# Optimization experiments

Hardware: AMD Instinct MI355X
Metric: run time of the kernel (lower is better)

Reference implementation:

```python
import jax, jax.numpy as jnp
import numpy as np

DIM = 3072
HEADS = 24
HEAD_DIM = 128
INNER = HEADS * HEAD_DIM
EPS = 1e-6
B, IMG_LEN, TXT_LEN = 1, 2048, 512
S = IMG_LEN + TXT_LEN


def setup_inputs() -> dict:
    key = jax.random.key(0)
    ks = jax.random.split(key, 16)
    w = lambda k, shp: (jax.random.normal(k, shp, dtype=jnp.float32) * 0.02)
    return {
        "x": jax.random.normal(ks[0], (B, IMG_LEN, DIM), dtype=jnp.float32),
        "ctx": jax.random.normal(ks[1], (B, TXT_LEN, DIM), dtype=jnp.float32),
        "rope_cos": jax.random.uniform(ks[2], (S, HEAD_DIM), dtype=jnp.float32),
        "rope_sin": jax.random.uniform(ks[3], (S, HEAD_DIM), dtype=jnp.float32),
        "wq": w(ks[4], (INNER, DIM)),
        "wk": w(ks[5], (INNER, DIM)),
        "wv": w(ks[6], (INNER, DIM)),
        "gq": jnp.ones((HEAD_DIM,), jnp.float32),
        "gk": jnp.ones((HEAD_DIM,), jnp.float32),
        "wo": w(ks[7], (DIM, INNER)),
        "awq": w(ks[8], (INNER, DIM)),
        "awk": w(ks[9], (INNER, DIM)),
        "awv": w(ks[10], (INNER, DIM)),
        "agq": jnp.ones((HEAD_DIM,), jnp.float32),
        "agk": jnp.ones((HEAD_DIM,), jnp.float32),
        "awo": w(ks[11], (DIM, INNER)),
    }


def _rms_norm(t, g):
    # t: [b, s, h, d]; normalize over last dim
    var = jnp.mean(t * t, axis=-1, keepdims=True)
    return t * jax.lax.rsqrt(var + EPS) * g


def _heads(t):
    # [b, s, h*d] -> [b, s, h, d]
    b, s, _ = t.shape
    return t.reshape(b, s, HEADS, HEAD_DIM)


def _apply_rope(t, cos, sin):
    # t: [b, s, h, d]; cos/sin: [s, d] interleaved-pair layout (diffusers Flux style)
    b, s, h, d = t.shape
    x = t.reshape(b, s, h, d // 2, 2)
    rot = jnp.stack([-x[..., 1], x[..., 0]], axis=-1).reshape(b, s, h, d)
    c = cos[None, :, None, :]
    si = sin[None, :, None, :]
    return t * c + rot * si


def reference(x, ctx, rope_cos, rope_sin, wq, wk, wv, gq, gk, wo,
              awq, awk, awv, agq, agk, awo):
    # image-stream QKV + per-head RMSNorm on q,k
    q = _rms_norm(_heads(x @ wq.T), gq)
    k = _rms_norm(_heads(x @ wk.T), gk)
    v = _heads(x @ wv.T)
    # context-stream QKV
    qc = _rms_norm(_heads(ctx @ awq.T), agq)
    kc = _rms_norm(_heads(ctx @ awk.T), agk)
    vc = _heads(ctx @ awv.T)
    # joint streams: [ctx, img] ordering (out[:, :txt_len] is context)
    q = jnp.concatenate([qc, q], axis=1)
    k = jnp.concatenate([kc, k], axis=1)
    v = jnp.concatenate([vc, v], axis=1)
    q = _apply_rope(q, rope_cos, rope_sin)
    k = _apply_rope(k, rope_cos, rope_sin)
    # SDPA
    scale = 1.0 / jnp.sqrt(jnp.float32(HEAD_DIM))
    scores = jnp.einsum('bqhd,bkhd->bhqk', q, k) * scale
    probs = jax.nn.softmax(scores, axis=-1)
    out = jnp.einsum('bhqk,bkhd->bqhd', probs, v)
    out = out.reshape(out.shape[0], out.shape[1], INNER)
    img_out = out[:, TXT_LEN:] @ wo.T
    txt_out = out[:, :TXT_LEN] @ awo.T
    return (img_out, txt_out)
```

## Files before the change

kernel.cpp:

```cpp
#include <hip/hip_runtime.h>
#include <hip/hip_bf16.h>

#define DIMC 3072
#define NHEADS 24
#define HD 128
#define SEQ 2560
#define TXTLEN 512
#define IMGLEN 2048

using short8 = __attribute__((ext_vector_type(8))) short;
using f32x4  = __attribute__((ext_vector_type(4))) float;

static __device__ __forceinline__ float bf2f(unsigned short u) {
    unsigned v = ((unsigned)u) << 16;
    return __builtin_bit_cast(float, v);
}
static __device__ __forceinline__ unsigned short f2bf(float f) {
    unsigned u = __builtin_bit_cast(unsigned, f);
    return (unsigned short)((u + 0x7FFFu + ((u >> 16) & 1u)) >> 16);
}
static __device__ __forceinline__ void gload16(const void* g, void* l) {
    __builtin_amdgcn_global_load_lds((const __attribute__((address_space(1))) unsigned int*)g,
                                     (__attribute__((address_space(3))) unsigned int*)l,
                                     16, 0, 0);
}

__global__ __launch_bounds__(256)
void castk(const float* __restrict__ in, unsigned short* __restrict__ out, int n8)
{
    const int i = blockIdx.x * 256 + threadIdx.x;
    if (i >= n8) return;
    const float4 a = *reinterpret_cast<const float4*>(in + (size_t)i * 8);
    const float4 b = *reinterpret_cast<const float4*>(in + (size_t)i * 8 + 4);
    short8 o;
    o[0] = (short)f2bf(a.x); o[1] = (short)f2bf(a.y);
    o[2] = (short)f2bf(a.z); o[3] = (short)f2bf(a.w);
    o[4] = (short)f2bf(b.x); o[5] = (short)f2bf(b.y);
    o[6] = (short)f2bf(b.z); o[7] = (short)f2bf(b.w);
    *reinterpret_cast<short8*>(out + (size_t)i * 8) = o;
}

struct W8 { const float* src[8]; };
__global__ __launch_bounds__(256)
void castw(W8 a, unsigned short* __restrict__ dstbase, int n8, size_t wsz)
{
    const int i = blockIdx.x * 256 + threadIdx.x;
    if (i >= n8) return;
    const float* in = a.src[blockIdx.y];
    unsigned short* out = dstbase + (size_t)blockIdx.y * wsz;
    const float4 av = *reinterpret_cast<const float4*>(in + (size_t)i * 8);
    const float4 bv = *reinterpret_cast<const float4*>(in + (size_t)i * 8 + 4);
    short8 o;
    o[0] = (short)f2bf(av.x); o[1] = (short)f2bf(av.y);
    o[2] = (short)f2bf(av.z); o[3] = (short)f2bf(av.w);
    o[4] = (short)f2bf(bv.x); o[5] = (short)f2bf(bv.y);
    o[6] = (short)f2bf(bv.z); o[7] = (short)f2bf(bv.w);
    *reinterpret_cast<short8*>(out + (size_t)i * 8) = o;
}

struct QkvArgs {
    const unsigned short* A;
    const unsigned short* w0[3];
    const unsigned short* w1[3];
    unsigned short* c[3];
    const float *gq, *gk, *agq, *agk, *rc, *rs;
};

__global__ __launch_bounds__(256)
void gemm_qkv(QkvArgs args)
{
    __shared__ unsigned short As[128 * 32];
    __shared__ unsigned short Bs[128 * 32];

    const int bm = blockIdx.x;
    int bn = blockIdx.y;
    const int which = bn / 24; bn -= which * 24;
    const int rowbase = bm * 128, colbase = bn * 128;
    const unsigned short* __restrict__ A = args.A;
    const unsigned short* __restrict__ W = (rowbase < TXTLEN) ? args.w0[which] : args.w1[which];
    unsigned short* __restrict__ C = args.c[which];

    const int t = threadIdx.x, w = t >> 6, l = t & 63;
    const int lr = l & 15, lk = l >> 4;

    f32x4 acc[2][8] = {};

    const unsigned short* Ag = A + (size_t)(rowbase + w * 32 + (l >> 2)) * DIMC + (l & 3) * 8;
    const unsigned short* Wg = W + (size_t)(colbase + w * 32 + (l >> 2)) * DIMC + (l & 3) * 8;
    unsigned short* AsB = &As[w * 1024];
    unsigned short* BsB = &Bs[w * 1024];

    for (int k0 = 0; k0 < DIMC; k0 += 32) {
        gload16(Ag + k0,             AsB);
        gload16(Ag + 16 * DIMC + k0, AsB + 512);
        gload16(Wg + k0,             BsB);
        gload16(Wg + 16 * DIMC + k0, BsB + 512);
        __syncthreads();
        short8 af[2], bf[8];
#pragma unroll
        for (int m = 0; m < 2; ++m)
            af[m] = *reinterpret_cast<const short8*>(&As[(w * 32 + m * 16 + lr) * 32 + lk * 8]);
#pragma unroll
        for (int n = 0; n < 8; ++n)
            bf[n] = *reinterpret_cast<const short8*>(&Bs[(n * 16 + lr) * 32 + lk * 8]);
#pragma unroll
        for (int m = 0; m < 2; ++m)
#pragma unroll
            for (int n = 0; n < 8; ++n)
                acc[m][n] = __builtin_amdgcn_mfma_f32_16x16x32_bf16(af[m], bf[n], acc[m][n], 0, 0, 0);
        __syncthreads();
    }

    if (which < 2) {
        const float* gg = (which == 0) ? ((rowbase < TXTLEN) ? args.agq : args.gq)
                                       : ((rowbase < TXTLEN) ? args.agk : args.gk);
        const float qscale = (which == 0) ? 0.08838834764831845f : 1.0f;
        float gcol[8];
#pragma unroll
        for (int n = 0; n < 8; ++n) gcol[n] = gg[n * 16 + lr];

#pragma unroll
        for (int m = 0; m < 2; ++m) {
#pragma unroll
            for (int r = 0; r < 4; ++r) {
                const int srow = rowbase + w * 32 + m * 16 + lk * 4 + r;
                float ss = 0.f;
#pragma unroll
                for (int n = 0; n < 8; ++n) ss += acc[m][n][r] * acc[m][n][r];
#pragma unroll
                for (int off = 1; off < 16; off <<= 1) ss += __shfl_xor(ss, off);
                const float rn = rsqrtf(ss * (1.f / HD) + 1e-6f);
                unsigned short* crow = C + (size_t)srow * DIMC + colbase;
                const float* crs = args.rc + (size_t)srow * HD;
                const float* srs = args.rs + (size_t)srow * HD;
#pragma unroll
                for (int n = 0; n < 8; ++n) {
                    const int col = n * 16 + lr;
                    const float v = acc[m][n][r] * rn * gcol[n];
                    const float pv = __shfl_xor(v, 1);
                    const float o = (v * crs[col] + ((lr & 1) ? pv : -pv) * srs[col]) * qscale;
                    crow[col] = f2bf(o);
                }
            }
        }
    } else {
#pragma unroll
        for (int m = 0; m < 2; ++m) {
#pragma unroll
            for (int r = 0; r < 4; ++r) {
                const int srow = rowbase + w * 32 + m * 16 + lk * 4 + r;
                unsigned short* crow = C + (size_t)srow * DIMC + colbase;
#pragma unroll
                for (int n = 0; n < 8; ++n)
                    crow[n * 16 + lr] = f2bf(acc[m][n][r]);
            }
        }
    }
}

__global__ __launch_bounds__(256)
void gemm_out(const unsigned short* __restrict__ A, const unsigned short* __restrict__ W0,
              const unsigned short* __restrict__ W1, float* __restrict__ Ctxt,
              float* __restrict__ Cimg)
{
    __shared__ unsigned short As[128 * 32];
    __shared__ unsigned short Bs[128 * 32];

    const int bm = blockIdx.x, bn = blockIdx.y;
    const int rowbase = bm * 128, colbase = bn * 128;
    const unsigned short* __restrict__ W = (rowbase < TXTLEN) ? W0 : W1;

    const int t = threadIdx.x, w = t >> 6, l = t & 63;
    const int lr = l & 15, lk = l >> 4;
    const int wr = (w >> 1) * 64, wc = (w & 1) * 64;

    f32x4 acc[4][4] = {};

    const unsigned short* Ag = A + (size_t)(rowbase + w * 32 + (l >> 2)) * DIMC + (l & 3) * 8;
    const unsigned short* Wg = W + (size_t)(colbase + w * 32 + (l >> 2)) * DIMC + (l & 3) * 8;
    unsigned short* AsB = &As[w * 1024];
    unsigned short* BsB = &Bs[w * 1024];

    for (int k0 = 0; k0 < DIMC; k0 += 32) {
        gload16(Ag + k0,             AsB);
        gload16(Ag + 16 * DIMC + k0, AsB + 512);
        gload16(Wg + k0,             BsB);
        gload16(Wg + 16 * DIMC + k0, BsB + 512);
        __syncthreads();
        short8 af[4], bf[4];
#pragma unroll
        for (int m = 0; m < 4; ++m)
            af[m] = *reinterpret_cast<const short8*>(&As[(wr + m * 16 + lr) * 32 + lk * 8]);
#pragma unroll
        for (int n = 0; n < 4; ++n)
            bf[n] = *reinterpret_cast<const short8*>(&Bs[(wc + n * 16 + lr) * 32 + lk * 8]);
#pragma unroll
        for (int m = 0; m < 4; ++m)
#pragma unroll
            for (int n = 0; n < 4; ++n)
                acc[m][n] = __builtin_amdgcn_mfma_f32_16x16x32_bf16(af[m], bf[n], acc[m][n], 0, 0, 0);
        __syncthreads();
    }

    float* Cb; int rloc;
    if (rowbase < TXTLEN) { Cb = Ctxt; rloc = rowbase; }
    else                  { Cb = Cimg; rloc = rowbase - TXTLEN; }
#pragma unroll
    for (int m = 0; m < 4; ++m) {
#pragma unroll
        for (int r = 0; r < 4; ++r) {
            const int row = rloc + wr + m * 16 + lk * 4 + r;
            float* crow = Cb + (size_t)row * DIMC + colbase + wc;
#pragma unroll
            for (int n = 0; n < 4; ++n)
                crow[n * 16 + lr] = acc[m][n][r];
        }
    }
}

__global__ __launch_bounds__(256)
void transpose_v(const unsigned short* __restrict__ V, unsigned short* __restrict__ Vt)
{
    __shared__ unsigned short Ts[64][136];
    const int kt = blockIdx.x, h = blockIdx.y;
    const int t = threadIdx.x;
#pragma unroll
    for (int p = 0; p < 4; ++p) {
        const int row = p * 16 + (t >> 4);
        const int col = (t & 15) * 8;
        *reinterpret_cast<short8*>(&Ts[row][col]) =
            *reinterpret_cast<const short8*>(V + (size_t)(kt * 64 + row) * DIMC + h * HD + col);
    }
    __syncthreads();
    const int d = t >> 1, kh = t & 1;
    unsigned short* dst = Vt + (size_t)h * HD * SEQ + (size_t)d * SEQ + kt * 64 + kh * 32;
#pragma unroll
    for (int j4 = 0; j4 < 4; ++j4) {
        short8 o;
#pragma unroll
        for (int j = 0; j < 8; ++j) o[j] = (short)Ts[kh * 32 + j4 * 8 + j][d];
        *reinterpret_cast<short8*>(dst + j4 * 8) = o;
    }
}

__global__ __launch_bounds__(512)
void attn_mfma(const unsigned short* __restrict__ Q, const unsigned short* __restrict__ K,
               const unsigned short* __restrict__ Vt, unsigned short* __restrict__ O)
{
    __shared__ unsigned short Ks[2][64 * 128];
    __shared__ unsigned short Vs[2][128 * 64];
    __shared__ unsigned short Ps[8][16 * 64];

    const int bq = blockIdx.x, h = blockIdx.y;
    const int t = threadIdx.x, w = t >> 6, l = t & 63;
    const int lr = l & 15, lk = l >> 4;
    const int q0 = bq * 128 + w * 16;

    short8 qf[4];
#pragma unroll
    for (int kk = 0; kk < 4; ++kk)
        qf[kk] = *reinterpret_cast<const short8*>(
            Q + (size_t)(q0 + lr) * DIMC + h * HD + kk * 32 + lk * 8);

    f32x4 oacc[8] = {};
    float mrow[4] = {-1e30f, -1e30f, -1e30f, -1e30f};
    float lrow[4] = {};

    const unsigned short* Kg[2];
    const unsigned short* Vg[2];
    int krow_[2], vrow_[2];
#pragma unroll
    for (int i = 0; i < 2; ++i) {
        const int kr = w * 8 + i * 4 + (l >> 4);
        krow_[i] = kr;
        Kg[i] = K + (size_t)kr * DIMC + h * HD + (((l & 15) ^ (kr & 7)) * 8);
        const int vr = w * 16 + i * 8 + (l >> 3);
        vrow_[i] = vr;
        Vg[i] = Vt + (size_t)h * HD * SEQ + (size_t)vr * SEQ + (((l & 7) ^ (vr & 7)) * 8);
    }

    auto STAGE = [&](int buf, int kv0) {
#pragma unroll
        for (int i = 0; i < 2; ++i) {
            gload16(Kg[i] + (size_t)kv0 * DIMC, &Ks[buf][(w * 8 + i * 4) * 128]);
            gload16(Vg[i] + kv0,                &Vs[buf][(w * 16 + i * 8) * 64]);
        }
    };

    STAGE(0, 0);

    constexpr int NT = SEQ / 64;
    for (int kt = 0; kt < NT; ++kt) {
        const int buf = kt & 1;
        __syncthreads();
        if (kt + 1 < NT) STAGE(buf ^ 1, (kt + 1) * 64);

        f32x4 sf[4] = {};
#pragma unroll
        for (int nf = 0; nf < 4; ++nf) {
            const int row = nf * 16 + lr;
            const int sw = (row & 7) << 3;
#pragma unroll
            for (int kk = 0; kk < 4; ++kk) {
                short8 bfr = *reinterpret_cast<const short8*>(
                    &Ks[buf][row * 128 + ((kk * 32 + lk * 8) ^ sw)]);
                sf[nf] = __builtin_amdgcn_mfma_f32_16x16x32_bf16(qf[kk], bfr, sf[nf], 0, 0, 0);
            }
        }

        float alpha[4];
#pragma unroll
        for (int r = 0; r < 4; ++r) {
            float mx = fmaxf(fmaxf(sf[0][r], sf[1][r]), fmaxf(sf[2][r], sf[3][r]));
#pragma unroll
            for (int off = 1; off < 16; off <<= 1) mx = fmaxf(mx, __shfl_xor(mx, off));
            const float mn = fmaxf(mrow[r], mx);
            alpha[r] = __expf(mrow[r] - mn);
            mrow[r] = mn;
            float ps = 0.f;
#pragma unroll
            for (int nf = 0; nf < 4; ++nf) {
                const float p = __expf(sf[nf][r] - mn);
                sf[nf][r] = p;
                ps += p;
            }
#pragma unroll
            for (int off = 1; off < 16; off <<= 1) ps += __shfl_xor(ps, off);
            lrow[r] = lrow[r] * alpha[r] + ps;
        }
#pragma unroll
        for (int nf = 0; nf < 8; ++nf)
#pragma unroll
            for (int r = 0; r < 4; ++r) oacc[nf][r] *= alpha[r];

#pragma unroll
        for (int r = 0; r < 4; ++r) {
            const int prow = lk * 4 + r;
            const int sw = (prow & 7) << 3;
#pragma unroll
            for (int nf = 0; nf < 4; ++nf) {
                const int col = nf * 16 + lr;
                Ps[w][prow * 64 + (col ^ sw)] = f2bf(sf[nf][r]);
            }
        }

#pragma unroll
        for (int ks = 0; ks < 2; ++ks) {
            short8 pa = *reinterpret_cast<const short8*>(
                &Ps[w][lr * 64 + ((ks * 32 + lk * 8) ^ ((lr & 7) << 3))]);
#pragma unroll
            for (int nf = 0; nf < 8; ++nf) {
                const int vrow = nf * 16 + lr;
                short8 vf = *reinterpret_cast<const short8*>(
                    &Vs[buf][vrow * 64 + ((ks * 32 + lk * 8) ^ ((vrow & 7) << 3))]);
                oacc[nf] = __builtin_amdgcn_mfma_f32_16x16x32_bf16(pa, vf, oacc[nf], 0, 0, 0);
            }
        }
    }

    float inv[4];
#pragma unroll
    for (int r = 0; r < 4; ++r) inv[r] = 1.f / lrow[r];
#pragma unroll
    for (int nf = 0; nf < 8; ++nf)
#pragma unroll
        for (int r = 0; r < 4; ++r)
            O[(size_t)(q0 + lk * 4 + r) * DIMC + h * HD + nf * 16 + lr] = f2bf(oacc[nf][r] * inv[r]);
}

extern "C" void kernel_launch(void* const* d_in, const int* in_sizes, int n_in,
                              void* d_out, int out_size, void* d_ws, size_t ws_size,
                              hipStream_t stream)
{
    const float* x    = (const float*)d_in[0];
    const float* ctx  = (const float*)d_in[1];
    const float* rc   = (const float*)d_in[2];
    const float* rs   = (const float*)d_in[3];
    const float* wq   = (const float*)d_in[4];
    const float* wk   = (const float*)d_in[5];
    const float* wv   = (const float*)d_in[6];
    const float* gq   = (const float*)d_in[7];
    const float* gk   = (const float*)d_in[8];
    const float* wo   = (const float*)d_in[9];
    const float* awq  = (const float*)d_in[10];
    const float* awk  = (const float*)d_in[11];
    const float* awv  = (const float*)d_in[12];
    const float* agq  = (const float*)d_in[13];
    const float* agk  = (const float*)d_in[14];
    const float* awo  = (const float*)d_in[15];

    unsigned short* wsp = (unsigned short*)d_ws;
    const size_t SZ  = (size_t)SEQ * DIMC;
    const size_t WSZ = (size_t)DIMC * DIMC;
    unsigned short* XC  = wsp;
    unsigned short* Qb  = XC + SZ;
    unsigned short* Kb  = Qb + SZ;
    unsigned short* Vb  = Kb + SZ;
    unsigned short* Vtb = Vb + SZ;
    unsigned short* Ob  = Vtb + SZ;
    unsigned short* Wc  = Ob + SZ;

    {
        int n8 = (int)((size_t)TXTLEN * DIMC / 8);
        castk<<<dim3((n8 + 255) / 256), dim3(256), 0, stream>>>(ctx, XC, n8);
        n8 = (int)((size_t)IMGLEN * DIMC / 8);
        castk<<<dim3((n8 + 255) / 256), dim3(256), 0, stream>>>(x, XC + (size_t)TXTLEN * DIMC, n8);
    }
    {
        W8 w8;
        w8.src[0] = awq; w8.src[1] = wq; w8.src[2] = awk; w8.src[3] = wk;
        w8.src[4] = awv; w8.src[5] = wv; w8.src[6] = awo; w8.src[7] = wo;
        const int n8 = (int)(WSZ / 8);
        castw<<<dim3((n8 + 255) / 256, 8), dim3(256), 0, stream>>>(w8, Wc, n8, WSZ);
    }

    QkvArgs qa;
    qa.A = XC;
    qa.w0[0] = Wc + 0 * WSZ; qa.w1[0] = Wc + 1 * WSZ; qa.c[0] = Qb;
    qa.w0[1] = Wc + 2 * WSZ; qa.w1[1] = Wc + 3 * WSZ; qa.c[1] = Kb;
    qa.w0[2] = Wc + 4 * WSZ; qa.w1[2] = Wc + 5 * WSZ; qa.c[2] = Vb;
    qa.gq = gq; qa.gk = gk; qa.agq = agq; qa.agk = agk; qa.rc = rc; qa.rs = rs;
    gemm_qkv<<<dim3(SEQ / 128, 72), dim3(256), 0, stream>>>(qa);

    transpose_v<<<dim3(SEQ / 64, NHEADS), dim3(256), 0, stream>>>(Vb, Vtb);

    attn_mfma<<<dim3(SEQ / 128, NHEADS), dim3(512), 0, stream>>>(Qb, Kb, Vtb, Ob);

    float* out = (float*)d_out;
    gemm_out<<<dim3(SEQ / 128, DIMC / 128), dim3(256), 0, stream>>>(
        Ob, Wc + 6 * WSZ, Wc + 7 * WSZ, out + (size_t)IMGLEN * DIMC, out);
}
```

Baseline: 642.9 us.

## Double-buffer GEMMs, swizzle block order, split norm/RoPE into separate kernel

Both GEMMs now use double-buffered LDS staging, issuing the next K-slice load before computing the current one, and drop one barrier per iteration. Launches become 1D grids with an XCD-aware swizzle of block indices to improve L2 locality. The QKV GEMM switches to a 2x2 warp tiling and moves per-head RMSNorm and RoPE into a new normrope kernel, which adds an extra read/write pass over Q and K. The attention kernel wraps its MFMA sections in s_setprio to favour matrix issue.

After: 588.6 us. 8.5% less time.

```diff
diff --git a/kernel.cpp b/kernel.cpp
--- a/kernel.cpp
+++ b/kernel.cpp
@@ -63,18 +63,20 @@
     const unsigned short* w0[3];
     const unsigned short* w1[3];
     unsigned short* c[3];
-    const float *gq, *gk, *agq, *agk, *rc, *rs;
 };
 
 __global__ __launch_bounds__(256)
 void gemm_qkv(QkvArgs args)
 {
-    __shared__ unsigned short As[128 * 32];
-    __shared__ unsigned short Bs[128 * 32];
-
-    const int bm = blockIdx.x;
-    int bn = blockIdx.y;
+    __shared__ unsigned short As[2][128 * 32];
+    __shared__ unsigned short Bs[2][128 * 32];
+
+    const int bid = blockIdx.x;
+    const int swz = (bid & 7) * 180 + (bid >> 3);
+    const int bm = swz % 20;
+    int bn = swz / 20;
     const int which = bn / 24; bn -= which * 24;
+
     const int rowbase = bm * 128, colbase = bn * 128;
     const unsigned short* __restrict__ A = args.A;
     const unsigned short* __restrict__ W = (rowbase < TXTLEN) ? args.w0[which] : args.w1[which];
@@ -82,78 +84,51 @@
 
     const int t = threadIdx.x, w = t >> 6, l = t & 63;
     const int lr = l & 15, lk = l >> 4;
-
-    f32x4 acc[2][8] = {};
+    const int wr = (w >> 1) * 64, wc = (w & 1) * 64;
+
+    f32x4 acc[4][4] = {};
 
     const unsigned short* Ag = A + (size_t)(rowbase + w * 32 + (l >> 2)) * DIMC + (l & 3) * 8;
     const unsigned short* Wg = W + (size_t)(colbase + w * 32 + (l >> 2)) * DIMC + (l & 3) * 8;
-    unsigned short* AsB = &As[w * 1024];
-    unsigned short* BsB = &Bs[w * 1024];
-
-    for (int k0 = 0; k0 < DIMC; k0 += 32) {
-        gload16(Ag + k0,             AsB);
-        gload16(Ag + 16 * DIMC + k0, AsB + 512);
-        gload16(Wg + k0,             BsB);
-        gload16(Wg + 16 * DIMC + k0, BsB + 512);
+
+    auto STAGE = [&](int buf, int k0) {
+        gload16(Ag + k0,             &As[buf][w * 1024]);
+        gload16(Ag + 16 * DIMC + k0, &As[buf][w * 1024 + 512]);
+        gload16(Wg + k0,             &Bs[buf][w * 1024]);
+        gload16(Wg + 16 * DIMC + k0, &Bs[buf][w * 1024 + 512]);
+    };
+
+    STAGE(0, 0);
+
+    constexpr int NIT = DIMC / 32;
+    for (int it = 0; it < NIT; ++it) {
+        const int buf = it & 1;
         __syncthreads();
-        short8 af[2], bf[8];
-#pragma unroll
-        for (int m = 0; m < 2; ++m)
-            af[m] = *reinterpret_cast<const short8*>(&As[(w * 32 + m * 16 + lr) * 32 + lk * 8]);
-#pragma unroll
-        for (int n = 0; n < 8; ++n)
-            bf[n] = *reinterpret_cast<const short8*>(&Bs[(n * 16 + lr) * 32 + lk * 8]);
-#pragma unroll
-        for (int m = 0; m < 2; ++m)
-#pragma unroll
-            for (int n = 0; n < 8; ++n)
+        if (it + 1 < NIT) STAGE(buf ^ 1, (it + 1) * 32);
+
+        short8 af[4], bf[4];
+#pragma unroll
+        for (int m = 0; m < 4; ++m)
+            af[m] = *reinterpret_cast<const short8*>(&As[buf][(wr + m * 16 + lr) * 32 + lk * 8]);
+#pragma unroll
+        for (int n = 0; n < 4; ++n)
+            bf[n] = *reinterpret_cast<const short8*>(&Bs[buf][(wc + n * 16 + lr) * 32 + lk * 8]);
+#pragma unroll
+        for (int m = 0; m < 4; ++m)
+#pragma unroll
+            for (int n = 0; n < 4; ++n)
                 acc[m][n] = __builtin_amdgcn_mfma_f32_16x16x32_bf16(af[m], bf[n], acc[m][n], 0, 0, 0);
-        __syncthreads();
-    }
-
-    if (which < 2) {
-        const float* gg = (which == 0) ? ((rowbase < TXTLEN) ? args.agq : args.gq)
-                                       : ((rowbase < TXTLEN) ? args.agk : args.gk);
-        const float qscale = (which == 0) ? 0.08838834764831845f : 1.0f;
-        float gcol[8];
-#pragma unroll
-        for (int n = 0; n < 8; ++n) gcol[n] = gg[n * 16 + lr];
-
-#pragma unroll
-        for (int m = 0; m < 2; ++m) {
-#pragma unroll
-            for (int r = 0; r < 4; ++r) {
-                const int srow = rowbase + w * 32 + m * 16 + lk * 4 + r;
-                float ss = 0.f;
-#pragma unroll
-                for (int n = 0; n < 8; ++n) ss += acc[m][n][r] * acc[m][n][r];
-#pragma unroll
-                for (int off = 1; off < 16; off <<= 1) ss += __shfl_xor(ss, off);
-                const float rn = rsqrtf(ss * (1.f / HD) + 1e-6f);
-                unsigned short* crow = C + (size_t)srow * DIMC + colbase;
-                const float* crs = args.rc + (size_t)srow * HD;
-                const float* srs = args.rs + (size_t)srow * HD;
-#pragma unroll
-                for (int n = 0; n < 8; ++n) {
-                    const int col = n * 16 + lr;
-                    const float v = acc[m][n][r] * rn * gcol[n];
-                    const float pv = __shfl_xor(v, 1);
-                    const float o = (v * crs[col] + ((lr & 1) ? pv : -pv) * srs[col]) * qscale;
-                    crow[col] = f2bf(o);
-                }
-            }
-        }
-    } else {
-#pragma unroll
-        for (int m = 0; m < 2; ++m) {
-#pragma unroll
-            for (int r = 0; r < 4; ++r) {
-                const int srow = rowbase + w * 32 + m * 16 + lk * 4 + r;
-                unsigned short* crow = C + (size_t)srow * DIMC + colbase;
-#pragma unroll
-                for (int n = 0; n < 8; ++n)
-                    crow[n * 16 + lr] = f2bf(acc[m][n][r]);
-            }
+    }
+
+#pragma unroll
+    for (int m = 0; m < 4; ++m) {
+#pragma unroll
+        for (int r = 0; r < 4; ++r) {
+            const int row = rowbase + wr + m * 16 + lk * 4 + r;
+            unsigned short* crow = C + (size_t)row * DIMC + colbase + wc;
+#pragma unroll
+            for (int n = 0; n < 4; ++n)
+                crow[n * 16 + lr] = f2bf(acc[m][n][r]);
         }
     }
 }
@@ -163,10 +138,14 @@
               const unsigned short* __restrict__ W1, float* __restrict__ Ctxt,
               float* __restrict__ Cimg)
 {
-    __shared__ unsigned short As[128 * 32];
-    __shared__ unsigned short Bs[128 * 32];
-
-    const int bm = blockIdx.x, bn = blockIdx.y;
+    __shared__ unsigned short As[2][128 * 32];
+    __shared__ unsigned short Bs[2][128 * 32];
+
+    const int bid = blockIdx.x;
+    const int swz = (bid & 7) * 60 + (bid >> 3);
+    const int bm = swz % 20;
+    const int bn = swz / 20;
+
     const int rowbase = bm * 128, colbase = bn * 128;
     const unsigned short* __restrict__ W = (rowbase < TXTLEN) ? W0 : W1;
 
@@ -178,28 +157,34 @@
 
     const unsigned short* Ag = A + (size_t)(rowbase + w * 32 + (l >> 2)) * DIMC + (l & 3) * 8;
     const unsigned short* Wg = W + (size_t)(colbase + w * 32 + (l >> 2)) * DIMC + (l & 3) * 8;
-    unsigned short* AsB = &As[w * 1024];
-    unsigned short* BsB = &Bs[w * 1024];
-
-    for (int k0 = 0; k0 < DIMC; k0 += 32) {
-        gload16(Ag + k0,             AsB);
-        gload16(Ag + 16 * DIMC + k0, AsB + 512);
-        gload16(Wg + k0,             BsB);
-        gload16(Wg + 16 * DIMC + k0, BsB + 512);
+
+    auto STAGE = [&](int buf, int k0) {
+        gload16(Ag + k0,             &As[buf][w * 1024]);
+        gload16(Ag + 16 * DIMC + k0, &As[buf][w * 1024 + 512]);
+        gload16(Wg + k0,             &Bs[buf][w * 1024]);
+        gload16(Wg + 16 * DIMC + k0, &Bs[buf][w * 1024 + 512]);
+    };
+
+    STAGE(0, 0);
+
+    constexpr int NIT = DIMC / 32;
+    for (int it = 0; it < NIT; ++it) {
+        const int buf = it & 1;
         __syncthreads();
+        if (it + 1 < NIT) STAGE(buf ^ 1, (it + 1) * 32);
+
         short8 af[4], bf[4];
 #pragma unroll
         for (int m = 0; m < 4; ++m)
-            af[m] = *reinterpret_cast<const short8*>(&As[(wr + m * 16 + lr) * 32 + lk * 8]);
+            af[m] = *reinterpret_cast<const short8*>(&As[buf][(wr + m * 16 + lr) * 32 + lk * 8]);
 #pragma unroll
         for (int n = 0; n < 4; ++n)
-            bf[n] = *reinterpret_cast<const short8*>(&Bs[(wc + n * 16 + lr) * 32 + lk * 8]);
+            bf[n] = *reinterpret_cast<const short8*>(&Bs[buf][(wc + n * 16 + lr) * 32 + lk * 8]);
 #pragma unroll
         for (int m = 0; m < 4; ++m)
 #pragma unroll
             for (int n = 0; n < 4; ++n)
                 acc[m][n] = __builtin_amdgcn_mfma_f32_16x16x32_bf16(af[m], bf[n], acc[m][n], 0, 0, 0);
-        __syncthreads();
     }
 
     float* Cb; int rloc;
@@ -215,6 +200,54 @@
             for (int n = 0; n < 4; ++n)
                 crow[n * 16 + lr] = acc[m][n][r];
         }
+    }
+}
+
+__global__ __launch_bounds__(256)
+void normrope(unsigned short* __restrict__ Q, unsigned short* __restrict__ K,
+              const float* __restrict__ gq, const float* __restrict__ gk,
+              const float* __restrict__ agq, const float* __restrict__ agk,
+              const float* __restrict__ rc, const float* __restrict__ rs)
+{
+    const int wid  = (blockIdx.x << 2) + (threadIdx.x >> 6);
+    const int lane = threadIdx.x & 63;
+    const int s = wid / NHEADS, h = wid - s * NHEADS;
+    const bool img = (s >= TXTLEN);
+    const float* gq_ = img ? gq : agq;
+    const float* gk_ = img ? gk : agk;
+
+    const size_t base = (size_t)s * DIMC + h * HD + lane * 2;
+    const float2 c2  = *reinterpret_cast<const float2*>(rc + (size_t)s * HD + lane * 2);
+    const float2 s2  = *reinterpret_cast<const float2*>(rs + (size_t)s * HD + lane * 2);
+    const float2 gqv = *reinterpret_cast<const float2*>(gq_ + lane * 2);
+    const float2 gkv = *reinterpret_cast<const float2*>(gk_ + lane * 2);
+
+    {
+        unsigned pr = *reinterpret_cast<unsigned*>(Q + base);
+        float vx = bf2f((unsigned short)(pr & 0xffff));
+        float vy = bf2f((unsigned short)(pr >> 16));
+        float ss = vx * vx + vy * vy;
+#pragma unroll
+        for (int off = 1; off < 64; off <<= 1) ss += __shfl_xor(ss, off);
+        const float rr = rsqrtf(ss * (1.f / HD) + 1e-6f);
+        const float txv = vx * rr * gqv.x, tyv = vy * rr * gqv.y;
+        const float qs = 0.08838834764831845f;
+        const float ox = (txv * c2.x - tyv * s2.x) * qs;
+        const float oy = (tyv * c2.y + txv * s2.y) * qs;
+        *reinterpret_cast<unsigned*>(Q + base) = (unsigned)f2bf(ox) | ((unsigned)f2bf(oy) << 16);
+    }
+    {
+        unsigned pr = *reinterpret_cast<unsigned*>(K + base);
+        float vx = bf2f((unsigned short)(pr & 0xffff));
+        float vy = bf2f((unsigned short)(pr >> 16));
+        float ss = vx * vx + vy * vy;
+#pragma unroll
+        for (int off = 1; off < 64; off <<= 1) ss += __shfl_xor(ss, off);
+        const float rr = rsqrtf(ss * (1.f / HD) + 1e-6f);
+        const float txv = vx * rr * gkv.x, tyv = vy * rr * gkv.y;
+        const float ox = txv * c2.x - tyv * s2.x;
+        const float oy = tyv * c2.y + txv * s2.y;
+        *reinterpret_cast<unsigned*>(K + base) = (unsigned)f2bf(ox) | ((unsigned)f2bf(oy) << 16);
     }
 }
 
@@ -268,14 +301,11 @@
 
     const unsigned short* Kg[2];
     const unsigned short* Vg[2];
-    int krow_[2], vrow_[2];
 #pragma unroll
     for (int i = 0; i < 2; ++i) {
         const int kr = w * 8 + i * 4 + (l >> 4);
-        krow_[i] = kr;
         Kg[i] = K + (size_t)kr * DIMC + h * HD + (((l & 15) ^ (kr & 7)) * 8);
         const int vr = w * 16 + i * 8 + (l >> 3);
-        vrow_[i] = vr;
         Vg[i] = Vt + (size_t)h * HD * SEQ + (size_t)vr * SEQ + (((l & 7) ^ (vr & 7)) * 8);
     }
 
@@ -296,6 +326,7 @@
         if (kt + 1 < NT) STAGE(buf ^ 1, (kt + 1) * 64);
 
         f32x4 sf[4] = {};
+        __builtin_amdgcn_s_setprio(1);
 #pragma unroll
         for (int nf = 0; nf < 4; ++nf) {
             const int row = nf * 16 + lr;
@@ -307,6 +338,7 @@
                 sf[nf] = __builtin_amdgcn_mfma_f32_16x16x32_bf16(qf[kk], bfr, sf[nf], 0, 0, 0);
             }
         }
+        __builtin_amdgcn_s_setprio(0);
 
         float alpha[4];
 #pragma unroll
@@ -344,6 +376,7 @@
             }
         }
 
+        __builtin_amdgcn_s_setprio(1);
 #pragma unroll
         for (int ks = 0; ks < 2; ++ks) {
             short8 pa = *reinterpret_cast<const short8*>(
@@ -356,6 +389,7 @@
                 oacc[nf] = __builtin_amdgcn_mfma_f32_16x16x32_bf16(pa, vf, oacc[nf], 0, 0, 0);
             }
         }
+        __builtin_amdgcn_s_setprio(0);
     }
 
     float inv[4];
@@ -419,14 +453,15 @@
     qa.w0[0] = Wc + 0 * WSZ; qa.w1[0] = Wc + 1 * WSZ; qa.c[0] = Qb;
     qa.w0[1] = Wc + 2 * WSZ; qa.w1[1] = Wc + 3 * WSZ; qa.c[1] = Kb;
     qa.w0[2] = Wc + 4 * WSZ; qa.w1[2] = Wc + 5 * WSZ; qa.c[2] = Vb;
-    qa.gq = gq; qa.gk = gk; qa.agq = agq; qa.agk = agk; qa.rc = rc; qa.rs = rs;
-    gemm_qkv<<<dim3(SEQ / 128, 72), dim3(256), 0, stream>>>(qa);
+    gemm_qkv<<<dim3(1440), dim3(256), 0, stream>>>(qa);
+
+    normrope<<<dim3(SEQ * NHEADS / 4), dim3(256), 0, stream>>>(Qb, Kb, gq, gk, agq, agk, rc, rs);
 
     transpose_v<<<dim3(SEQ / 64, NHEADS), dim3(256), 0, stream>>>(Vb, Vtb);
 
     attn_mfma<<<dim3(SEQ / 128, NHEADS), dim3(512), 0, stream>>>(Qb, Kb, Vtb, Ob);
 
     float* out = (float*)d_out;
-    gemm_out<<<dim3(SEQ / 128, DIMC / 128), dim3(256), 0, stream>>>(
+    gemm_out<<<dim3(480), dim3(256), 0, stream>>>(
         Ob, Wc + 6 * WSZ, Wc + 7 * WSZ, out + (size_t)IMGLEN * DIMC, out);
 }
```
